# Optimization experiments

Measured on AMD Instinct MI355X. Metric: run time of the kernel, lower is better.

## Reference

```python
import jax, jax.numpy as jnp
import numpy as np

N_NODES = 50000
N_EDGES = 800000
D_IN = 256
N_HEADS = 8
D_OUT = 32
NEG_SLOPE = 0.2


def setup_inputs() -> dict:
    key = jax.random.key(0)
    k1, k2, k3, k4, k5, k6 = jax.random.split(key, 6)
    feat = jax.random.normal(k1, (N_NODES, D_IN), dtype=jnp.float32)
    # xavier-ish scale for projection weight
    W = jax.random.normal(k2, (D_IN, N_HEADS * D_OUT), dtype=jnp.float32) * (2.0 / (D_IN + N_HEADS * D_OUT)) ** 0.5
    attn_l = jax.random.normal(k3, (N_HEADS, D_OUT), dtype=jnp.float32) * 0.1
    attn_r = jax.random.normal(k4, (N_HEADS, D_OUT), dtype=jnp.float32) * 0.1
    src = jax.random.randint(k5, (N_EDGES,), 0, N_NODES, dtype=jnp.int32)
    dst = jax.random.randint(k6, (N_EDGES,), 0, N_NODES, dtype=jnp.int32)
    return {"feat": feat, "W": W, "attn_l": attn_l, "attn_r": attn_r, "src": src, "dst": dst}


def reference(feat, W, attn_l, attn_r, src, dst):
    # Linear projection: [N, D_in] @ [D_in, H*D] -> [N, H, D]
    feat_proj = (feat @ W).reshape(-1, N_HEADS, D_OUT)
    # Per-node attention logits (el for src role, er for dst role): [N, H]
    el = jnp.einsum("nhd,hd->nh", feat_proj, attn_l)
    er = jnp.einsum("nhd,hd->nh", feat_proj, attn_r)
    # Edge scores: LeakyReLU(el[u] + er[v]), shape [E, H]
    e = el[src] + er[dst]
    e = jnp.where(e > 0, e, NEG_SLOPE * e)
    # Edge softmax normalized over incoming edges of each dst node
    emax = jax.ops.segment_max(e, dst, num_segments=N_NODES)  # [N, H], -inf for isolated dst
    emax = jnp.where(jnp.isfinite(emax), emax, 0.0)
    ee = jnp.exp(e - emax[dst])
    esum = jax.ops.segment_sum(ee, dst, num_segments=N_NODES)  # [N, H]
    a = ee / jnp.where(esum == 0, 1.0, esum)[dst]              # [E, H]
    # Weighted gather-scatter aggregation: sum_j a_ij * Wh_j -> [N, H, D]
    msgs = a[:, :, None] * feat_proj[src]
    rst = jax.ops.segment_sum(msgs, dst, num_segments=N_NODES)
    return rst
```

## Files before the change

kernel.cpp:

```cpp
#include <hip/hip_runtime.h>
#include <math.h>
#include <stdint.h>

#define D_IN 256
#define NH 8
#define DOUT 32
#define NOUT 256
#define NEG_SLOPE 0.2f
#define AST 264
#define BINW 128

typedef short bf16x8 __attribute__((ext_vector_type(8)));
typedef float f32x4 __attribute__((ext_vector_type(4)));
typedef unsigned short u16x4 __attribute__((ext_vector_type(4)));

__device__ __forceinline__ short bf16_rne(float f) {
    uint32_t x = __float_as_uint(f);
    uint32_t r = (x + 0x7FFFu + ((x >> 16) & 1u)) >> 16;
    return (short)(uint16_t)r;
}
__device__ __forceinline__ float bf16_to_f(short h) {
    return __uint_as_float(((uint32_t)(uint16_t)h) << 16);
}
__device__ __forceinline__ float bfu_to_f(unsigned short h) {
    return __uint_as_float(((uint32_t)h) << 16);
}

__global__ __launch_bounds__(256) void prep_kernel(const float* __restrict__ W,
                                                   short* __restrict__ Bth,
                                                   const int* __restrict__ src,
                                                   const int* __restrict__ dst,
                                                   int* __restrict__ cnt,
                                                   unsigned short* __restrict__ bins, int E) {
    int b = blockIdx.x;
    if (b < NOUT) {
        int n = b, k = threadIdx.x;
        Bth[(size_t)n * D_IN + k] = bf16_rne(W[(size_t)k * NOUT + n]);
    } else {
        int i = (b - NOUT) * 256 + threadIdx.x;
        if (i < E) {
            int d = dst[i];
            int slot = atomicAdd(&cnt[d], 1);
            if (slot < BINW) bins[(size_t)d * BINW + slot] = (unsigned short)src[i];
        }
    }
}

__global__ __launch_bounds__(512, 2) void gemm_mfma_kernel(const float* __restrict__ A,
                                                           const short* __restrict__ Bth,
                                                           const float* __restrict__ attn_l,
                                                           const float* __restrict__ attn_r,
                                                           short* __restrict__ projh,
                                                           float* __restrict__ el,
                                                           float* __restrict__ er, int M) {
    __shared__ short Ah[2][16][AST];
    int tid = threadIdx.x;
    int w = tid >> 6, lane = tid & 63;
    int l15 = lane & 15, l4 = lane >> 4;
    int ntiles = (M + 15) >> 4;

    bf16x8 bfr[2][8];
    {
        const short* bb = Bth + (size_t)(w * 32 + l15) * D_IN + l4 * 8;
#pragma unroll
        for (int ct = 0; ct < 2; ++ct)
#pragma unroll
            for (int kb = 0; kb < 8; ++kb)
                bfr[ct][kb] = *reinterpret_cast<const bf16x8*>(
                    bb + (size_t)ct * 16 * D_IN + kb * 32);
    }
    float alc0 = attn_l[w * 32 + l15], alc1 = attn_l[w * 32 + 16 + l15];
    float arc0 = attn_r[w * 32 + l15], arc1 = attn_r[w * 32 + 16 + l15];

    int srow = tid >> 5;
    int sj = (tid & 31) * 8;

    int t0 = blockIdx.x;
    {
        int arow = t0 * 16 + srow;
        float4 v0 = make_float4(0.f, 0.f, 0.f, 0.f), v1 = v0;
        if (arow < M) {
            const float* ap = A + (size_t)arow * D_IN + sj;
            v0 = *reinterpret_cast<const float4*>(ap);
            v1 = *reinterpret_cast<const float4*>(ap + 4);
        }
        float f[8] = {v0.x, v0.y, v0.z, v0.w, v1.x, v1.y, v1.z, v1.w};
        bf16x8 h;
#pragma unroll
        for (int j = 0; j < 8; ++j) h[j] = bf16_rne(f[j]);
        *reinterpret_cast<bf16x8*>(&Ah[0][srow][sj]) = h;
    }
    __syncthreads();

    int it = 0;
    for (int t = t0; t < ntiles; t += gridDim.x, ++it) {
        int buf = it & 1;
        int tn = t + gridDim.x;
        if (tn < ntiles) {
            int arow = tn * 16 + srow;
            float4 v0 = make_float4(0.f, 0.f, 0.f, 0.f), v1 = v0;
            if (arow < M) {
                const float* ap = A + (size_t)arow * D_IN + sj;
                v0 = *reinterpret_cast<const float4*>(ap);
                v1 = *reinterpret_cast<const float4*>(ap + 4);
            }
            float f[8] = {v0.x, v0.y, v0.z, v0.w, v1.x, v1.y, v1.z, v1.w};
            bf16x8 h;
#pragma unroll
            for (int j = 0; j < 8; ++j) h[j] = bf16_rne(f[j]);
            *reinterpret_cast<bf16x8*>(&Ah[buf ^ 1][srow][sj]) = h;
        }
        f32x4 acc0 = {0.f, 0.f, 0.f, 0.f}, acc1 = acc0;
#pragma unroll
        for (int kb = 0; kb < 8; ++kb) {
            bf16x8 a_h = *reinterpret_cast<const bf16x8*>(&Ah[buf][l15][kb * 32 + l4 * 8]);
            acc0 = __builtin_amdgcn_mfma_f32_16x16x32_bf16(a_h, bfr[0][kb], acc0, 0, 0, 0);
            acc1 = __builtin_amdgcn_mfma_f32_16x16x32_bf16(a_h, bfr[1][kb], acc1, 0, 0, 0);
        }
#pragma unroll
        for (int r = 0; r < 4; ++r) {
            int row = t * 16 + l4 * 4 + r;
            bool ok = row < M;
            if (ok) {
                projh[(size_t)row * NOUT + w * 32 + l15] = bf16_rne(acc0[r]);
                projh[(size_t)row * NOUT + w * 32 + 16 + l15] = bf16_rne(acc1[r]);
            }
            float ev = acc0[r] * alc0 + acc1[r] * alc1;
            float ee = acc0[r] * arc0 + acc1[r] * arc1;
#pragma unroll
            for (int s = 1; s < 16; s <<= 1) {
                ev += __shfl_xor(ev, s, 64);
                ee += __shfl_xor(ee, s, 64);
            }
            if (l15 == 0 && ok) {
                el[(size_t)row * NH + w] = ev;
                er[(size_t)row * NH + w] = ee;
            }
        }
        __syncthreads();
    }
}

__global__ __launch_bounds__(256) void agg_kernel(const unsigned short* __restrict__ projh,
                                                  const float* __restrict__ el,
                                                  const float* __restrict__ er,
                                                  const unsigned short* __restrict__ bins,
                                                  const int* __restrict__ cnt,
                                                  float* __restrict__ out, int N) {
    __shared__ float pS[4][64][NH + 1];
    __shared__ int uS[4][64];
    int w = threadIdx.x >> 6, lane = threadIdx.x & 63;
    int v = blockIdx.x * 4 + w;
    if (v >= N) return;
    int n = min(cnt[v], BINW);
    const unsigned short* csrU = bins + (size_t)v * BINW;
    float4 acc = make_float4(0.f, 0.f, 0.f, 0.f);
    int h4 = lane >> 3;

    if (n > 0) {
        const float4* el4 = reinterpret_cast<const float4*>(el);
        const float4* er4 = reinterpret_cast<const float4*>(er);
        float4 e0 = er4[(size_t)v * 2], e1 = er4[(size_t)v * 2 + 1];
        float er_r[NH] = {e0.x, e0.y, e0.z, e0.w, e1.x, e1.y, e1.z, e1.w};

        if (n <= 64) {
            int u_reg = 0;
            float p[NH], sm[NH];
            bool act = lane < n;
            if (act) {
                u_reg = csrU[lane];
                float4 a0 = el4[(size_t)u_reg * 2], a1 = el4[(size_t)u_reg * 2 + 1];
                float xin[NH] = {a0.x, a0.y, a0.z, a0.w, a1.x, a1.y, a1.z, a1.w};
#pragma unroll
                for (int h = 0; h < NH; ++h) {
                    float t = xin[h] + er_r[h];
                    t = (t > 0.f) ? t : NEG_SLOPE * t;
                    p[h] = __expf(t);
                }
            } else {
#pragma unroll
                for (int h = 0; h < NH; ++h) p[h] = 0.f;
            }
#pragma unroll
            for (int h = 0; h < NH; ++h) sm[h] = p[h];
#pragma unroll
            for (int s = 32; s; s >>= 1)
#pragma unroll
                for (int h = 0; h < NH; ++h) sm[h] += __shfl_xor(sm[h], s, 64);
#pragma unroll
            for (int h = 0; h < NH; ++h) pS[w][lane][h] = p[h] * (1.f / sm[h]);
            __builtin_amdgcn_wave_barrier();

            int kk = 0;
            for (; kk + 8 <= n; kk += 8) {
#pragma unroll
                for (int j = 0; j < 8; ++j) {
                    int u = __shfl(u_reg, kk + j, 64);
                    float pp = pS[w][kk + j][h4];
                    u16x4 vv = *reinterpret_cast<const u16x4*>(&projh[(size_t)u * NOUT + lane * 4]);
                    acc.x += pp * bfu_to_f(vv[0]);
                    acc.y += pp * bfu_to_f(vv[1]);
                    acc.z += pp * bfu_to_f(vv[2]);
                    acc.w += pp * bfu_to_f(vv[3]);
                }
            }
            for (; kk < n; ++kk) {
                int u = __shfl(u_reg, kk, 64);
                float pp = pS[w][kk][h4];
                u16x4 vv = *reinterpret_cast<const u16x4*>(&projh[(size_t)u * NOUT + lane * 4]);
                acc.x += pp * bfu_to_f(vv[0]);
                acc.y += pp * bfu_to_f(vv[1]);
                acc.z += pp * bfu_to_f(vv[2]);
                acc.w += pp * bfu_to_f(vv[3]);
            }
        } else {
            float sm[NH] = {};
            for (int c0 = 0; c0 < n; c0 += 64) {
                if (lane < n - c0) {
                    int u = csrU[c0 + lane];
                    float4 a0 = el4[(size_t)u * 2], a1 = el4[(size_t)u * 2 + 1];
                    float xin[NH] = {a0.x, a0.y, a0.z, a0.w, a1.x, a1.y, a1.z, a1.w};
#pragma unroll
                    for (int h = 0; h < NH; ++h) {
                        float t = xin[h] + er_r[h];
                        t = (t > 0.f) ? t : NEG_SLOPE * t;
                        sm[h] += __expf(t);
                    }
                }
            }
#pragma unroll
            for (int s = 32; s; s >>= 1)
#pragma unroll
                for (int h = 0; h < NH; ++h) sm[h] += __shfl_xor(sm[h], s, 64);
            float inv[NH];
#pragma unroll
            for (int h = 0; h < NH; ++h) inv[h] = 1.f / sm[h];
            for (int c0 = 0; c0 < n; c0 += 64) {
                int cn = min(64, n - c0);
                if (lane < cn) {
                    int u = csrU[c0 + lane];
                    uS[w][lane] = u;
                    float4 a0 = el4[(size_t)u * 2], a1 = el4[(size_t)u * 2 + 1];
                    float xin[NH] = {a0.x, a0.y, a0.z, a0.w, a1.x, a1.y, a1.z, a1.w};
#pragma unroll
                    for (int h = 0; h < NH; ++h) {
                        float t = xin[h] + er_r[h];
                        t = (t > 0.f) ? t : NEG_SLOPE * t;
                        pS[w][lane][h] = __expf(t) * inv[h];
                    }
                }
                __builtin_amdgcn_wave_barrier();
                for (int k = 0; k < cn; ++k) {
                    int u = uS[w][k];
                    float pp = pS[w][k][h4];
                    u16x4 vv = *reinterpret_cast<const u16x4*>(&projh[(size_t)u * NOUT + lane * 4]);
                    acc.x += pp * bfu_to_f(vv[0]);
                    acc.y += pp * bfu_to_f(vv[1]);
                    acc.z += pp * bfu_to_f(vv[2]);
                    acc.w += pp * bfu_to_f(vv[3]);
                }
                __builtin_amdgcn_wave_barrier();
            }
        }
    }
    *reinterpret_cast<float4*>(&out[(size_t)v * NOUT + lane * 4]) = acc;
}

extern "C" void kernel_launch(void* const* d_in, const int* in_sizes, int n_in,
                              void* d_out, int out_size, void* d_ws, size_t ws_size,
                              hipStream_t stream) {
    const float* feat   = (const float*)d_in[0];
    const float* W      = (const float*)d_in[1];
    const float* attn_l = (const float*)d_in[2];
    const float* attn_r = (const float*)d_in[3];
    const int*   src    = (const int*)d_in[4];
    const int*   dst    = (const int*)d_in[5];
    float* out = (float*)d_out;

    const int M = in_sizes[0] / D_IN;
    const int E = in_sizes[4];

    char* ws = (char*)d_ws;
    size_t o = 0;
    auto alloc = [&](size_t bytes) { size_t r = o; o = (o + bytes + 255) & ~(size_t)255; return r; };
    size_t off_projh = alloc((size_t)M * NOUT * 2);
    size_t off_el    = alloc((size_t)M * NH * 4);
    size_t off_er    = alloc((size_t)M * NH * 4);
    size_t off_cnt   = alloc((size_t)M * 4);
    size_t off_bins  = alloc((size_t)M * BINW * 2);
    size_t off_bth   = alloc((size_t)D_IN * NOUT * 2);

    unsigned short* projh = (unsigned short*)(ws + off_projh);
    float* el   = (float*)(ws + off_el);
    float* er   = (float*)(ws + off_er);
    int*   cnt  = (int*)(ws + off_cnt);
    unsigned short* bins = (unsigned short*)(ws + off_bins);
    short* bth  = (short*)(ws + off_bth);

    hipMemsetAsync(cnt, 0, (size_t)M * 4, stream);

    int eblocks = (E + 255) / 256;
    prep_kernel<<<NOUT + eblocks, 256, 0, stream>>>(W, bth, src, dst, cnt, bins, E);

    gemm_mfma_kernel<<<1024, 512, 0, stream>>>(feat, bth, attn_l, attn_r,
                                               (short*)projh, el, er, M);

    agg_kernel<<<(M + 3) / 4, 256, 0, stream>>>(projh, el, er, bins, cnt, out, M);
}
```

Measured before the change: 163.4 us.

## Fuse edge binning into GEMM kernel, enlarge agg blocks, trim softmax shuffles

Moves the dst-binning atomics out of the prep kernel into the start of the MFMA GEMM kernel as a grid-stride loop. The W transpose now runs alone in a small kernel. The goal is to overlap the atomic scatter with the GEMM work and shrink the prep kernel. The aggregation kernel now uses 1024-thread blocks holding 16 nodes each, and the softmax sum reduction only runs shuffle steps up to the next power of two above the degree. The shortened reduction is still correct because inactive lanes contribute zero. The cost is that the GEMM kernel's tail now carries atomic latency before its main loop, and the agg kernel needs more shared memory per block.

```diff
diff --git a/kernel.cpp b/kernel.cpp
--- a/kernel.cpp
+++ b/kernel.cpp
@@ -26,35 +26,28 @@
     return __uint_as_float(((uint32_t)h) << 16);
 }
 
-__global__ __launch_bounds__(256) void prep_kernel(const float* __restrict__ W,
-                                                   short* __restrict__ Bth,
-                                                   const int* __restrict__ src,
-                                                   const int* __restrict__ dst,
-                                                   int* __restrict__ cnt,
-                                                   unsigned short* __restrict__ bins, int E) {
-    int b = blockIdx.x;
-    if (b < NOUT) {
-        int n = b, k = threadIdx.x;
-        Bth[(size_t)n * D_IN + k] = bf16_rne(W[(size_t)k * NOUT + n]);
-    } else {
-        int i = (b - NOUT) * 256 + threadIdx.x;
-        if (i < E) {
-            int d = dst[i];
-            int slot = atomicAdd(&cnt[d], 1);
-            if (slot < BINW) bins[(size_t)d * BINW + slot] = (unsigned short)src[i];
-        }
-    }
-}
-
-__global__ __launch_bounds__(512, 2) void gemm_mfma_kernel(const float* __restrict__ A,
-                                                           const short* __restrict__ Bth,
-                                                           const float* __restrict__ attn_l,
-                                                           const float* __restrict__ attn_r,
-                                                           short* __restrict__ projh,
-                                                           float* __restrict__ el,
-                                                           float* __restrict__ er, int M) {
+__global__ __launch_bounds__(256) void wprep_kernel(const float* __restrict__ W,
+                                                    short* __restrict__ Bth) {
+    int n = blockIdx.x, k = threadIdx.x;
+    Bth[(size_t)n * D_IN + k] = bf16_rne(W[(size_t)k * NOUT + n]);
+}
+
+__global__ __launch_bounds__(512, 2) void gemm_mfma_kernel(
+    const float* __restrict__ A, const short* __restrict__ Bth,
+    const int* __restrict__ src, const int* __restrict__ dst,
+    int* __restrict__ cnt, unsigned short* __restrict__ bins,
+    const float* __restrict__ attn_l, const float* __restrict__ attn_r,
+    short* __restrict__ projh, float* __restrict__ el, float* __restrict__ er,
+    int M, int E) {
     __shared__ short Ah[2][16][AST];
     int tid = threadIdx.x;
+
+    for (int i = blockIdx.x * 512 + tid; i < E; i += gridDim.x * 512) {
+        int d = dst[i];
+        int slot = atomicAdd(&cnt[d], 1);
+        if (slot < BINW) bins[(size_t)d * BINW + slot] = (unsigned short)src[i];
+    }
+
     int w = tid >> 6, lane = tid & 63;
     int l15 = lane & 15, l4 = lane >> 4;
     int ntiles = (M + 15) >> 4;
@@ -141,16 +134,16 @@
     }
 }
 
-__global__ __launch_bounds__(256) void agg_kernel(const unsigned short* __restrict__ projh,
-                                                  const float* __restrict__ el,
-                                                  const float* __restrict__ er,
-                                                  const unsigned short* __restrict__ bins,
-                                                  const int* __restrict__ cnt,
-                                                  float* __restrict__ out, int N) {
-    __shared__ float pS[4][64][NH + 1];
-    __shared__ int uS[4][64];
+__global__ __launch_bounds__(1024) void agg_kernel(const unsigned short* __restrict__ projh,
+                                                   const float* __restrict__ el,
+                                                   const float* __restrict__ er,
+                                                   const unsigned short* __restrict__ bins,
+                                                   const int* __restrict__ cnt,
+                                                   float* __restrict__ out, int N) {
+    __shared__ float pS[16][64][NH + 1];
+    __shared__ int uS[16][64];
     int w = threadIdx.x >> 6, lane = threadIdx.x & 63;
-    int v = blockIdx.x * 4 + w;
+    int v = blockIdx.x * 16 + w;
     if (v >= N) return;
     int n = min(cnt[v], BINW);
     const unsigned short* csrU = bins + (size_t)v * BINW;
@@ -183,8 +176,9 @@
             }
 #pragma unroll
             for (int h = 0; h < NH; ++h) sm[h] = p[h];
-#pragma unroll
-            for (int s = 32; s; s >>= 1)
+            int s0 = 1;
+            while (s0 < n) s0 <<= 1;
+            for (int s = s0 >> 1; s; s >>= 1)
 #pragma unroll
                 for (int h = 0; h < NH; ++h) sm[h] += __shfl_xor(sm[h], s, 64);
 #pragma unroll
@@ -299,11 +293,11 @@
 
     hipMemsetAsync(cnt, 0, (size_t)M * 4, stream);
 
-    int eblocks = (E + 255) / 256;
-    prep_kernel<<<NOUT + eblocks, 256, 0, stream>>>(W, bth, src, dst, cnt, bins, E);
-
-    gemm_mfma_kernel<<<1024, 512, 0, stream>>>(feat, bth, attn_l, attn_r,
-                                               (short*)projh, el, er, M);
-
-    agg_kernel<<<(M + 3) / 4, 256, 0, stream>>>(projh, el, er, bins, cnt, out, M);
-}
+    wprep_kernel<<<NOUT, D_IN, 0, stream>>>(W, bth);
+
+    gemm_mfma_kernel<<<1024, 512, 0, stream>>>(feat, bth, src, dst, cnt, bins,
+                                               attn_l, attn_r,
+                                               (short*)projh, el, er, M, E);
+
+    agg_kernel<<<(M + 15) / 16, 1024, 0, stream>>>(projh, el, er, bins, cnt, out, M);
+}
```

Result: slower. 174.7 us (+6.9%).
